# Performance work log

Hardware: AMD Instinct MI355X
Metric: run time of the kernel (lower is better)

## Reference

```python
import jax, jax.numpy as jnp
import numpy as np
import math

B, H, S, D = 2, 8, 1024, 384
LAMBDA_INIT = 0.8 - 0.6 * math.exp(-0.3 * 1)  # depth = 1


def _clin(xr, xi, wr, wi, br=None, bi=None):
    # complex linear: (xr + i xi) @ (wr + i wi)^T + (br + i bi)
    o_r = jnp.einsum('bhse,de->bhsd', xr, wr) - jnp.einsum('bhse,de->bhsd', xi, wi)
    o_i = jnp.einsum('bhse,de->bhsd', xr, wi) + jnp.einsum('bhse,de->bhsd', xi, wr)
    if br is not None:
        o_r = o_r + br
        o_i = o_i + bi
    return o_r, o_i


def _attn_w(qr, qi, kr, ki, scale):
    # complex score magnitude -> softmax
    s_r = jnp.einsum('bhqd,bhkd->bhqk', qr, kr) + jnp.einsum('bhqd,bhkd->bhqk', qi, ki)
    s_i = jnp.einsum('bhqd,bhkd->bhqk', qi, kr) - jnp.einsum('bhqd,bhkd->bhqk', qr, ki)
    return jax.nn.softmax(jnp.sqrt(s_r ** 2 + s_i ** 2 + 1e-8) * scale, axis=-1)


def setup_inputs() -> dict:
    key = jax.random.key(0)
    ks = jax.random.split(key, 32)
    n = lambda k, sh, std=1.0: jax.random.normal(k, sh, dtype=jnp.float32) * std
    sd = 1.0 / math.sqrt(D)
    inp = {
        'q_r': n(ks[0], (B, H, S, D)), 'q_i': n(ks[1], (B, H, S, D)),
        'k_r': n(ks[2], (B, H, S, D)), 'k_i': n(ks[3], (B, H, S, D)),
        'v_r': n(ks[4], (B, H, S, D)), 'v_i': n(ks[5], (B, H, S, D)),
        'pe_q_r': n(ks[6], (B, H, S, D)), 'pe_q_i': n(ks[7], (B, H, S, D)),
        'pe_k_r': n(ks[8], (B, H, S, D)), 'pe_k_i': n(ks[9], (B, H, S, D)),
        'wq_r': n(ks[10], (2 * D, D), sd), 'wq_i': n(ks[11], (2 * D, D), sd),
        'bq_r': jnp.zeros((2 * D,), jnp.float32), 'bq_i': jnp.zeros((2 * D,), jnp.float32),
        'wk_r': n(ks[12], (D, D), sd), 'wk_i': n(ks[13], (D, D), sd),
        'bk_r': jnp.zeros((D,), jnp.float32), 'bk_i': jnp.zeros((D,), jnp.float32),
        'wv_r': n(ks[14], (D, D), sd), 'wv_i': n(ks[15], (D, D), sd),
        'bv_r': jnp.zeros((D,), jnp.float32), 'bv_i': jnp.zeros((D,), jnp.float32),
        'wg_r': n(ks[16], (D, D), sd), 'wg_i': n(ks[17], (D, D), sd),
        'bg_r': jnp.zeros((D,), jnp.float32), 'bg_i': jnp.zeros((D,), jnp.float32),
        'wo_r': n(ks[18], (D, D), sd), 'wo_i': n(ks[19], (D, D), sd),
        'bo_r': jnp.zeros((D,), jnp.float32), 'bo_i': jnp.zeros((D,), jnp.float32),
        'lam_q1': n(ks[20], (D,), 0.1), 'lam_k1': n(ks[21], (D,), 0.1),
        'lam_q2': n(ks[22], (D,), 0.1), 'lam_k2': n(ks[23], (D,), 0.1),
        'subln_w': jnp.ones((2 * D,), jnp.float32),
    }
    return inp


def reference(q_r, q_i, k_r, k_i, v_r, v_i, pe_q_r, pe_q_i, pe_k_r, pe_k_i,
              wq_r, wq_i, bq_r, bq_i, wk_r, wk_i, bk_r, bk_i,
              wv_r, wv_i, bv_r, bv_i, wg_r, wg_i, bg_r, bg_i,
              wo_r, wo_i, bo_r, bo_i, lam_q1, lam_k1, lam_q2, lam_k2, subln_w):
    scale = D ** (-0.5)
    qp_r, qp_i = _clin(q_r, q_i, wq_r, wq_i, bq_r, bq_i)   # [B,H,S,2D]
    kp_r, kp_i = _clin(k_r, k_i, wk_r, wk_i, bk_r, bk_i)   # [B,H,S,D]
    vp_r, vp_i = _clin(v_r, v_i, wv_r, wv_i, bv_r, bv_i)
    qp_r = qp_r + jnp.concatenate([pe_q_r, pe_q_r], axis=-1)
    qp_i = qp_i + jnp.concatenate([pe_q_i, pe_q_i], axis=-1)
    kp_r = kp_r + pe_k_r
    kp_i = kp_i + pe_k_i
    q1_r, q2_r = jnp.split(qp_r, 2, axis=-1)
    q1_i, q2_i = jnp.split(qp_i, 2, axis=-1)
    w1 = _attn_w(q1_r, q1_i, kp_r, kp_i, scale)
    w2 = _attn_w(q2_r, q2_i, kp_r, kp_i, scale)
    a1_r = jnp.einsum('bhqk,bhkd->bhqd', w1, vp_r)
    a1_i = jnp.einsum('bhqk,bhkd->bhqd', w1, vp_i)
    a2_r = jnp.einsum('bhqk,bhkd->bhqd', w2, vp_r)
    a2_i = jnp.einsum('bhqk,bhkd->bhqd', w2, vp_i)
    cat_r = jnp.concatenate([a1_r, a2_r], axis=-1)
    cat_i = jnp.concatenate([a1_i, a2_i], axis=-1)
    # complex RMSNorm (SubLN) over 2D dim
    rms = jnp.sqrt(jnp.mean(cat_r ** 2 + cat_i ** 2, axis=-1, keepdims=True) + 1e-5)
    cat_r = cat_r / rms * subln_w
    cat_i = cat_i / rms * subln_w
    a1_r, a2_r = jnp.split(cat_r, 2, axis=-1)
    a1_i, a2_i = jnp.split(cat_i, 2, axis=-1)
    lam1 = jnp.exp(jnp.sum(lam_q1 * lam_k1))
    lam2 = jnp.exp(jnp.sum(lam_q2 * lam_k2))
    lam = jax.nn.sigmoid(lam1 - lam2 + LAMBDA_INIT)
    out_r = a1_r - lam * a2_r
    out_i = a1_i - lam * a2_i
    g_r, g_i = _clin(q_r, q_i, wg_r, wg_i, bg_r, bg_i)
    out_r, out_i = g_r * out_r - g_i * out_i, g_r * out_i + g_i * out_r
    out_r, out_i = _clin(out_r, out_i, wo_r, wo_i, bo_r, bo_i)
    return (out_r, out_i)
```

## Files before the change

kernel.cpp:

```cpp
#include <hip/hip_runtime.h>
#include <cstdint>


typedef _Float16 f16;
typedef __attribute__((ext_vector_type(8))) _Float16 f16x8;
typedef __attribute__((ext_vector_type(4))) float    f32x4;

#define NROW      16384L
#define HALF_OUT  6291456L
#define SCALE_QK  0.05103103630798288f
#define LAMBDA_INIT 0.35550906759096926f

__device__ __forceinline__ void gl2lds16(const void* g, void* l) {
  __builtin_amdgcn_global_load_lds(
      (const __attribute__((address_space(1))) void*)(uintptr_t)g,
      (__attribute__((address_space(3))) void*)(uint32_t)(uintptr_t)l,
      16, 0, 0);
}

struct PeTab { const float* p[6]; float sgn[6]; };

enum { MODE_PROJ = 0, MODE_VT = 1, MODE_OUT = 2 };

template <int MODE, int BN>
__launch_bounds__(256, 2)
__global__ void gemm_kernel(const f16* __restrict__ A, int lda,
                            const f16* __restrict__ W, int ldw,
                            const float* __restrict__ bias, PeTab pe,
                            void* __restrict__ outp, int ldo, int K)
{
  constexpr int NT = BN / 32;
  __shared__ f16 As[2][128 * 32];
  __shared__ f16 Bs[2][BN * 32];
  const int t    = threadIdx.x;
  const int lane = t & 63;
  const int wave = t >> 6;
  const long row0 = (long)blockIdx.y * 128;
  const long col0 = (long)blockIdx.x * BN;
  const f16* Ab = A + row0 * (long)lda;
  const f16* Wb = W + col0 * (long)ldw;

  const int wm = (wave >> 1) * 64;
  const int wn = (wave & 1) * (BN / 2);
  const int lm = lane & 15;
  const int lk = (lane >> 4) * 8;

  f32x4 acc[4][NT] = {};

  auto stage = [&](int kk, int buf) {
#pragma unroll
    for (int j = 0; j < 2; ++j) {
      int sg = j * 256 + t, r = sg >> 2, c = (sg & 3) << 3;
      gl2lds16(Ab + (long)r * lda + kk + c, &As[buf][sg * 8]);
    }
#pragma unroll
    for (int j = 0; j < BN / 64; ++j) {
      int sg = j * 256 + t, r = sg >> 2, c = (sg & 3) << 3;
      gl2lds16(Wb + (long)r * ldw + kk + c, &Bs[buf][sg * 8]);
    }
  };

  stage(0, 0);
  __syncthreads();
  int buf = 0;
  for (int kk = 0; kk < K; kk += 32, buf ^= 1) {
    if (kk + 32 < K) stage(kk + 32, buf ^ 1);
    f16x8 bfr[NT];
#pragma unroll
    for (int nt = 0; nt < NT; ++nt)
      bfr[nt] = *(const f16x8*)&Bs[buf][(wn + nt * 16 + lm) * 32 + lk];
#pragma unroll
    for (int mt = 0; mt < 4; ++mt) {
      f16x8 afr = *(const f16x8*)&As[buf][(wm + mt * 16 + lm) * 32 + lk];
#pragma unroll
      for (int nt = 0; nt < NT; ++nt)
        acc[mt][nt] = __builtin_amdgcn_mfma_f32_16x16x32_f16(afr, bfr[nt], acc[mt][nt], 0, 0, 0);
    }
    __syncthreads();
  }

  const int lm4 = (lane >> 4) * 4;
  const int ln  = lane & 15;
#pragma unroll
  for (int mt = 0; mt < 4; ++mt) {
#pragma unroll
    for (int nt = 0; nt < NT; ++nt) {
      int col = (int)col0 + wn + nt * 16 + ln;
#pragma unroll
      for (int r = 0; r < 4; ++r) {
        long row = row0 + wm + mt * 16 + lm4 + r;
        float c = acc[mt][nt][r];
        if (MODE == MODE_PROJ) {
          c += bias[col];
          int s2 = col / 384;
          int d  = col - s2 * 384;
          const float* pp = pe.p[s2];
          if (pp) c += pe.sgn[s2] * pp[row * 384 + d];
          ((f16*)outp)[row * (long)ldo + col] = (f16)c;
        } else if (MODE == MODE_VT) {
          c += bias[col];
          long bh = row >> 10, sx = row & 1023;
          ((f16*)outp)[(bh * 768 + col) * 1024 + sx] = (f16)c;
        } else {
          c += bias[col];
          float* of = (float*)outp;
          if (col < 384) of[row * 384 + col] = c;
          else           of[HALF_OUT + row * 384 + (col - 384)] = c;
        }
      }
    }
  }
}

__launch_bounds__(256, 2)
__global__ void score_kernel(const f16* __restrict__ QG, const f16* __restrict__ Kc,
                             f16* __restrict__ P)
{
  __shared__ f16 AsL[2][128 * 32], AsH[2][128 * 32];
  __shared__ f16 BsL[2][128 * 32], BsH[2][128 * 32];
  const int t = threadIdx.x, lane = t & 63, wave = t >> 6;
  const int z = blockIdx.z, w = z >> 4, bh = z & 15;
  const long row0 = (long)blockIdx.y * 128, col0 = (long)blockIdx.x * 128;
  const f16* A = QG + (long)bh * 1024 * 2304 + row0 * 2304 + w * 768;
  const f16* B = Kc + (long)bh * 1024 * 768 + col0 * 768;
  f16* Pz = P + (long)z * 1024 * 1024;

  const int wm = (wave >> 1) * 64, wn = (wave & 1) * 64;
  const int lm = lane & 15, lk = (lane >> 4) * 8;
  f32x4 accr[4][4] = {}, acci[4][4] = {};

  auto stage = [&](int kk, int buf) {
#pragma unroll
    for (int j = 0; j < 2; ++j) {
      int sg = j * 256 + t, r = sg >> 2, c = (sg & 3) << 3;
      gl2lds16(A + (long)r * 2304 + kk + c,       &AsL[buf][sg * 8]);
      gl2lds16(A + (long)r * 2304 + 384 + kk + c, &AsH[buf][sg * 8]);
      gl2lds16(B + (long)r * 768 + kk + c,        &BsL[buf][sg * 8]);
      gl2lds16(B + (long)r * 768 + 384 + kk + c,  &BsH[buf][sg * 8]);
    }
  };

  stage(0, 0);
  __syncthreads();
  int buf = 0;
  for (int kk = 0; kk < 384; kk += 32, buf ^= 1) {
    if (kk + 32 < 384) stage(kk + 32, buf ^ 1);
    f16x8 bl[4], bh2[4];
#pragma unroll
    for (int nt = 0; nt < 4; ++nt) {
      bl[nt]  = *(const f16x8*)&BsL[buf][(wn + nt * 16 + lm) * 32 + lk];
      bh2[nt] = *(const f16x8*)&BsH[buf][(wn + nt * 16 + lm) * 32 + lk];
    }
#pragma unroll
    for (int mt = 0; mt < 4; ++mt) {
      f16x8 al  = *(const f16x8*)&AsL[buf][(wm + mt * 16 + lm) * 32 + lk];
      f16x8 ah  = *(const f16x8*)&AsH[buf][(wm + mt * 16 + lm) * 32 + lk];
      f16x8 nal = -al;
#pragma unroll
      for (int nt = 0; nt < 4; ++nt) {
        accr[mt][nt] = __builtin_amdgcn_mfma_f32_16x16x32_f16(al,  bl[nt],  accr[mt][nt], 0, 0, 0);
        accr[mt][nt] = __builtin_amdgcn_mfma_f32_16x16x32_f16(ah,  bh2[nt], accr[mt][nt], 0, 0, 0);
        acci[mt][nt] = __builtin_amdgcn_mfma_f32_16x16x32_f16(ah,  bl[nt],  acci[mt][nt], 0, 0, 0);
        acci[mt][nt] = __builtin_amdgcn_mfma_f32_16x16x32_f16(nal, bh2[nt], acci[mt][nt], 0, 0, 0);
      }
    }
    __syncthreads();
  }
  const int lm4 = (lane >> 4) * 4, ln = lane & 15;
#pragma unroll
  for (int mt = 0; mt < 4; ++mt)
#pragma unroll
    for (int nt = 0; nt < 4; ++nt) {
      int col = (int)col0 + wn + nt * 16 + ln;
#pragma unroll
      for (int r = 0; r < 4; ++r) {
        long row = row0 + wm + mt * 16 + lm4 + r;
        float sr = accr[mt][nt][r], si = acci[mt][nt][r];
        float m = sqrtf(sr * sr + si * si + 1e-8f) * SCALE_QK;
        Pz[row * 1024 + col] = (f16)m;
      }
    }
}

__launch_bounds__(256, 2)
__global__ void pv_kernel(const f16* __restrict__ P, const f16* __restrict__ Vt,
                          f16* __restrict__ O1, f16* __restrict__ O2)
{
  __shared__ f16 As1[2][128 * 32], As2[2][128 * 32], Bs[2][128 * 32];
  const int t = threadIdx.x, lane = t & 63, wave = t >> 6;
  const int bh = blockIdx.z;
  const long row0 = (long)blockIdx.y * 128, col0 = (long)blockIdx.x * 128;
  const f16* A1 = P + ((long)bh << 20) + row0 * 1024;
  const f16* A2 = P + ((long)(16 + bh) << 20) + row0 * 1024;
  const f16* B  = Vt + (long)bh * 768 * 1024 + col0 * 1024;

  const int wm = (wave >> 1) * 64, wn = (wave & 1) * 64;
  const int lm = lane & 15, lk = (lane >> 4) * 8;
  f32x4 ac1[4][4] = {}, ac2[4][4] = {};

  auto stage = [&](int kk, int buf) {
#pragma unroll
    for (int j = 0; j < 2; ++j) {
      int sg = j * 256 + t, r = sg >> 2, c = (sg & 3) << 3;
      gl2lds16(A1 + (long)r * 1024 + kk + c, &As1[buf][sg * 8]);
      gl2lds16(A2 + (long)r * 1024 + kk + c, &As2[buf][sg * 8]);
      gl2lds16(B  + (long)r * 1024 + kk + c, &Bs[buf][sg * 8]);
    }
  };

  stage(0, 0);
  __syncthreads();
  int buf = 0;
  for (int kk = 0; kk < 1024; kk += 32, buf ^= 1) {
    if (kk + 32 < 1024) stage(kk + 32, buf ^ 1);
    f16x8 bfr[4];
#pragma unroll
    for (int nt = 0; nt < 4; ++nt)
      bfr[nt] = *(const f16x8*)&Bs[buf][(wn + nt * 16 + lm) * 32 + lk];
#pragma unroll
    for (int mt = 0; mt < 4; ++mt) {
      f16x8 a1 = *(const f16x8*)&As1[buf][(wm + mt * 16 + lm) * 32 + lk];
      f16x8 a2 = *(const f16x8*)&As2[buf][(wm + mt * 16 + lm) * 32 + lk];
#pragma unroll
      for (int nt = 0; nt < 4; ++nt) {
        ac1[mt][nt] = __builtin_amdgcn_mfma_f32_16x16x32_f16(a1, bfr[nt], ac1[mt][nt], 0, 0, 0);
        ac2[mt][nt] = __builtin_amdgcn_mfma_f32_16x16x32_f16(a2, bfr[nt], ac2[mt][nt], 0, 0, 0);
      }
    }
    __syncthreads();
  }
  const int lm4 = (lane >> 4) * 4, ln = lane & 15;
#pragma unroll
  for (int mt = 0; mt < 4; ++mt)
#pragma unroll
    for (int nt = 0; nt < 4; ++nt) {
      int col = (int)col0 + wn + nt * 16 + ln;
#pragma unroll
      for (int r = 0; r < 4; ++r) {
        long row = (long)bh * 1024 + row0 + wm + mt * 16 + lm4 + r;
        O1[row * 768 + col] = (f16)ac1[mt][nt][r];
        O2[row * 768 + col] = (f16)ac2[mt][nt][r];
      }
    }
}

__global__ void softmax_kernel(f16* __restrict__ P)
{
  const long row = blockIdx.x;
  f16* p = P + row * 1024;
  const int lane = threadIdx.x;
  f16x8 v0 = *(const f16x8*)(p + lane * 16);
  f16x8 v1 = *(const f16x8*)(p + lane * 16 + 8);
  float x[16];
#pragma unroll
  for (int i = 0; i < 8; ++i) { x[i] = (float)v0[i]; x[8 + i] = (float)v1[i]; }
  float m = x[0];
#pragma unroll
  for (int i = 1; i < 16; ++i) m = fmaxf(m, x[i]);
#pragma unroll
  for (int off = 1; off < 64; off <<= 1) m = fmaxf(m, __shfl_xor(m, off));
  float s = 0.f;
#pragma unroll
  for (int i = 0; i < 16; ++i) { x[i] = __expf(x[i] - m); s += x[i]; }
#pragma unroll
  for (int off = 1; off < 64; off <<= 1) s += __shfl_xor(s, off);
  float inv = 1.f / s;
  f16x8 o0, o1;
#pragma unroll
  for (int i = 0; i < 8; ++i) { o0[i] = (f16)(x[i] * inv); o1[i] = (f16)(x[8 + i] * inv); }
  *(f16x8*)(p + lane * 16)     = o0;
  *(f16x8*)(p + lane * 16 + 8) = o1;
}

__global__ void fuse_kernel(const f16* __restrict__ A1, const f16* __restrict__ A2,
                            const f16* __restrict__ QG, const float* __restrict__ subw,
                            const float* __restrict__ lamp, f16* __restrict__ Xatt)
{
  const long row = blockIdx.x;
  const int t = threadIdx.x, lane = t & 63, wv = t >> 6;
  const f16* a1 = A1 + row * 768;
  const f16* a2 = A2 + row * 768;
  const f16* g  = QG + row * 2304 + 1536;
  float a1r[3], a1i[3], a2r[3], a2i[3];
  float ss = 0.f;
#pragma unroll
  for (int q = 0; q < 3; ++q) {
    int d = t + q * 128;
    a1r[q] = (float)a1[d]; a1i[q] = (float)a1[d + 384];
    a2r[q] = (float)a2[d]; a2i[q] = (float)a2[d + 384];
    ss += a1r[q] * a1r[q] + a1i[q] * a1i[q] + a2r[q] * a2r[q] + a2i[q] * a2i[q];
  }
#pragma unroll
  for (int m = 1; m < 64; m <<= 1) ss += __shfl_xor(ss, m);
  __shared__ float part[2];
  if (lane == 0) part[wv] = ss;
  __syncthreads();
  float inv = rsqrtf((part[0] + part[1]) * (1.f / 768.f) + 1e-5f);
  float lam = lamp[0];
#pragma unroll
  for (int q = 0; q < 3; ++q) {
    int d = t + q * 128;
    float w1 = subw[d], w2 = subw[d + 384];
    float n1r = a1r[q] * inv * w1, n1i = a1i[q] * inv * w1;
    float n2r = a2r[q] * inv * w2, n2i = a2i[q] * inv * w2;
    float orr = n1r - lam * n2r, oii = n1i - lam * n2i;
    float gr = (float)g[d], gi = (float)g[d + 384];
    Xatt[row * 768 + d]       = (f16)(gr * orr - gi * oii);
    Xatt[row * 768 + d + 384] = (f16)(gr * oii + gi * orr);
  }
}

__global__ void lam_kernel(const float* lq1, const float* lk1,
                           const float* lq2, const float* lk2, float* out)
{
  const int t = threadIdx.x, lane = t & 63, wv = t >> 6;
  float s1 = 0.f, s2 = 0.f;
#pragma unroll
  for (int q = 0; q < 3; ++q) {
    int d = t + q * 128;
    s1 += lq1[d] * lk1[d];
    s2 += lq2[d] * lk2[d];
  }
#pragma unroll
  for (int m = 1; m < 64; m <<= 1) { s1 += __shfl_xor(s1, m); s2 += __shfl_xor(s2, m); }
  __shared__ float p1[2], p2[2];
  if (lane == 0) { p1[wv] = s1; p2[wv] = s2; }
  __syncthreads();
  if (t == 0) {
    float x = expf(p1[0] + p1[1]) - expf(p2[0] + p2[1]) + LAMBDA_INIT;
    out[0] = 1.f / (1.f + expf(-x));
  }
}

__global__ void pack_x(const float* __restrict__ xr, const float* __restrict__ xi,
                       f16* __restrict__ X)
{
  long i = (long)blockIdx.x * 256 + threadIdx.x;
  long row = i / 768;
  int  c   = (int)(i - row * 768);
  float v = (c < 384) ? xr[row * 384 + c] : xi[row * 384 + (c - 384)];
  X[i] = (f16)v;
}

__global__ void pack_wq(const float* wq_r, const float* wq_i,
                        const float* wg_r, const float* wg_i,
                        const float* bq_r, const float* bq_i,
                        const float* bg_r, const float* bg_i,
                        f16* __restrict__ Wp, float* __restrict__ bp)
{
  long i = (long)blockIdx.x * 256 + threadIdx.x;
  int n = (int)(i / 768), e = (int)(i % 768);
  int s = n / 384, d = n - s * 384;
  int hb = (e >= 384);
  int ee = e - hb * 384;
  float v = 0.f, b = 0.f;
  switch (s) {
    case 0: v = hb ? -wq_i[d * 384 + ee]         :  wq_r[d * 384 + ee];         b = bq_r[d];       break;
    case 1: v = hb ?  wq_r[d * 384 + ee]         :  wq_i[d * 384 + ee];         b = bq_i[d];       break;
    case 2: v = hb ? -wq_i[(384 + d) * 384 + ee] :  wq_r[(384 + d) * 384 + ee]; b = bq_r[384 + d]; break;
    case 3: v = hb ?  wq_r[(384 + d) * 384 + ee] :  wq_i[(384 + d) * 384 + ee]; b = bq_i[384 + d]; break;
    case 4: v = hb ? -wg_i[d * 384 + ee]         :  wg_r[d * 384 + ee];         b = bg_r[d];       break;
    case 5: v = hb ?  wg_r[d * 384 + ee]         :  wg_i[d * 384 + ee];         b = bg_i[d];       break;
  }
  Wp[i] = (f16)v;
  if (e == 0) bp[n] = b;
}

__global__ void pack_w_std(const float* wr, const float* wi,
                           const float* br, const float* bi,
                           f16* __restrict__ Wp, float* __restrict__ bp)
{
  long i = (long)blockIdx.x * 256 + threadIdx.x;
  int n = (int)(i / 768), e = (int)(i % 768);
  int hb = (e >= 384);
  int ee = e - hb * 384;
  float v, b;
  if (n < 384) { v = hb ? -wi[n * 384 + ee] : wr[n * 384 + ee]; b = br[n]; }
  else { int d = n - 384; v = hb ? wr[d * 384 + ee] : wi[d * 384 + ee]; b = bi[d]; }
  Wp[i] = (f16)v;
  if (e == 0) bp[n] = b;
}

extern "C" void kernel_launch(void* const* d_in, const int* in_sizes, int n_in,
                              void* d_out, int out_size, void* d_ws, size_t ws_size,
                              hipStream_t stream)
{
  const float* q_r    = (const float*)d_in[0];
  const float* q_i    = (const float*)d_in[1];
  const float* k_r    = (const float*)d_in[2];
  const float* k_i    = (const float*)d_in[3];
  const float* v_r    = (const float*)d_in[4];
  const float* v_i    = (const float*)d_in[5];
  const float* pe_q_r = (const float*)d_in[6];
  const float* pe_q_i = (const float*)d_in[7];
  const float* pe_k_r = (const float*)d_in[8];
  const float* pe_k_i = (const float*)d_in[9];
  const float* wq_r = (const float*)d_in[10];
  const float* wq_i = (const float*)d_in[11];
  const float* bq_r = (const float*)d_in[12];
  const float* bq_i = (const float*)d_in[13];
  const float* wk_r = (const float*)d_in[14];
  const float* wk_i = (const float*)d_in[15];
  const float* bk_r = (const float*)d_in[16];
  const float* bk_i = (const float*)d_in[17];
  const float* wv_r = (const float*)d_in[18];
  const float* wv_i = (const float*)d_in[19];
  const float* bv_r = (const float*)d_in[20];
  const float* bv_i = (const float*)d_in[21];
  const float* wg_r = (const float*)d_in[22];
  const float* wg_i = (const float*)d_in[23];
  const float* bg_r = (const float*)d_in[24];
  const float* bg_i = (const float*)d_in[25];
  const float* wo_r = (const float*)d_in[26];
  const float* wo_i = (const float*)d_in[27];
  const float* bo_r = (const float*)d_in[28];
  const float* bo_i = (const float*)d_in[29];
  const float* lam_q1 = (const float*)d_in[30];
  const float* lam_k1 = (const float*)d_in[31];
  const float* lam_q2 = (const float*)d_in[32];
  const float* lam_k2 = (const float*)d_in[33];
  const float* subln_w = (const float*)d_in[34];

  char* base = (char*)d_ws;
  size_t off = 0;
  auto alloc = [&](size_t bytes) -> void* {
    void* p = base + off;
    off = (off + bytes + 255) & ~(size_t)255;
    return p;
  };
  f16*   Wq   = (f16*)alloc(2304L * 768 * 2);
  f16*   Wk   = (f16*)alloc(768L * 768 * 2);
  f16*   Wv   = (f16*)alloc(768L * 768 * 2);
  f16*   Wo   = (f16*)alloc(768L * 768 * 2);
  float* bq   = (float*)alloc(2304 * 4);
  float* bk   = (float*)alloc(768 * 4);
  float* bv   = (float*)alloc(768 * 4);
  float* bo   = (float*)alloc(768 * 4);
  float* lamp = (float*)alloc(4);
  f16*   X    = (f16*)alloc(NROW * 768 * 2);
  f16*   QG   = (f16*)alloc(NROW * 2304 * 2);
  f16*   Kc   = (f16*)alloc(NROW * 768 * 2);
  f16*   Vt   = (f16*)alloc(16L * 768 * 1024 * 2);
  f16*   P    = (f16*)alloc(32L * 1024 * 1024 * 2);
  if (off > ws_size) return;
  f16* A1   = Kc;
  f16* A2   = X;
  f16* Xatt = Vt;

  pack_wq<<<6912, 256, 0, stream>>>(wq_r, wq_i, wg_r, wg_i, bq_r, bq_i, bg_r, bg_i, Wq, bq);
  pack_w_std<<<2304, 256, 0, stream>>>(wk_r, wk_i, bk_r, bk_i, Wk, bk);
  pack_w_std<<<2304, 256, 0, stream>>>(wv_r, wv_i, bv_r, bv_i, Wv, bv);
  pack_w_std<<<2304, 256, 0, stream>>>(wo_r, wo_i, bo_r, bo_i, Wo, bo);
  lam_kernel<<<1, 128, 0, stream>>>(lam_q1, lam_k1, lam_q2, lam_k2, lamp);

  PeTab pe0{};

  pack_x<<<49152, 256, 0, stream>>>(q_r, q_i, X);
  PeTab peQ{};
  peQ.p[0] = pe_q_r; peQ.sgn[0] = 1.f;
  peQ.p[1] = pe_q_i; peQ.sgn[1] = 1.f;
  peQ.p[2] = pe_q_r; peQ.sgn[2] = 1.f;
  peQ.p[3] = pe_q_i; peQ.sgn[3] = 1.f;
  gemm_kernel<MODE_PROJ, 256><<<dim3(9, 128), 256, 0, stream>>>(
      X, 768, Wq, 768, bq, peQ, QG, 2304, 768);

  pack_x<<<49152, 256, 0, stream>>>(k_r, k_i, X);
  PeTab peK{};
  peK.p[0] = pe_k_r; peK.sgn[0] = 1.f;
  peK.p[1] = pe_k_i; peK.sgn[1] = 1.f;
  gemm_kernel<MODE_PROJ, 128><<<dim3(6, 128), 256, 0, stream>>>(
      X, 768, Wk, 768, bk, peK, Kc, 768, 768);

  pack_x<<<49152, 256, 0, stream>>>(v_r, v_i, X);
  gemm_kernel<MODE_VT, 128><<<dim3(6, 128), 256, 0, stream>>>(
      X, 768, Wv, 768, bv, pe0, Vt, 0, 768);

  score_kernel<<<dim3(8, 8, 32), 256, 0, stream>>>(QG, Kc, P);
  softmax_kernel<<<32768, 64, 0, stream>>>(P);
  pv_kernel<<<dim3(6, 8, 16), 256, 0, stream>>>(P, Vt, A1, A2);

  fuse_kernel<<<16384, 128, 0, stream>>>(A1, A2, QG, subln_w, lamp, Xatt);

  gemm_kernel<MODE_OUT, 128><<<dim3(6, 128), 256, 0, stream>>>(
      Xatt, 768, Wo, 768, bo, pe0, d_out, 0, 768);

  (void)in_sizes; (void)n_in; (void)out_size;
}
```

Baseline: 900.3 us.

## Remap GEMM blocks to XCDs for L2 locality and restructure K-loop staging

After: 833.8 us. 7.4% less time.

```diff
diff --git a/kernel.cpp b/kernel.cpp
--- a/kernel.cpp
+++ b/kernel.cpp
@@ -4,6 +4,7 @@
 
 typedef _Float16 f16;
 typedef __attribute__((ext_vector_type(8))) _Float16 f16x8;
+typedef __attribute__((ext_vector_type(4))) _Float16 f16x4;
 typedef __attribute__((ext_vector_type(4))) float    f32x4;
 
 #define NROW      16384L
@@ -22,59 +23,59 @@
 
 enum { MODE_PROJ = 0, MODE_VT = 1, MODE_OUT = 2 };
 
-template <int MODE, int BN>
+template <int MODE>
 __launch_bounds__(256, 2)
 __global__ void gemm_kernel(const f16* __restrict__ A, int lda,
                             const f16* __restrict__ W, int ldw,
                             const float* __restrict__ bias, PeTab pe,
-                            void* __restrict__ outp, int ldo, int K)
-{
-  constexpr int NT = BN / 32;
+                            void* __restrict__ outp, int ldo, int K, int gx)
+{
   __shared__ f16 As[2][128 * 32];
-  __shared__ f16 Bs[2][BN * 32];
+  __shared__ f16 Bs[2][128 * 32];
   const int t    = threadIdx.x;
   const int lane = t & 63;
   const int wave = t >> 6;
-  const long row0 = (long)blockIdx.y * 128;
-  const long col0 = (long)blockIdx.x * BN;
+  const int bid  = blockIdx.x;
+  const int xcd  = bid & 7;
+  const int per  = bid >> 3;
+  const long row0 = (long)(xcd * 16 + per / gx) * 128;
+  const long col0 = (long)(per % gx) * 128;
   const f16* Ab = A + row0 * (long)lda;
   const f16* Wb = W + col0 * (long)ldw;
 
   const int wm = (wave >> 1) * 64;
-  const int wn = (wave & 1) * (BN / 2);
+  const int wn = (wave & 1) * 64;
   const int lm = lane & 15;
   const int lk = (lane >> 4) * 8;
 
-  f32x4 acc[4][NT] = {};
-
-  auto stage = [&](int kk, int buf) {
+  f32x4 acc[4][4] = {};
+
+  auto stage = [&](int kk, int sub) {
 #pragma unroll
     for (int j = 0; j < 2; ++j) {
       int sg = j * 256 + t, r = sg >> 2, c = (sg & 3) << 3;
-      gl2lds16(Ab + (long)r * lda + kk + c, &As[buf][sg * 8]);
-    }
-#pragma unroll
-    for (int j = 0; j < BN / 64; ++j) {
-      int sg = j * 256 + t, r = sg >> 2, c = (sg & 3) << 3;
-      gl2lds16(Wb + (long)r * ldw + kk + c, &Bs[buf][sg * 8]);
+      gl2lds16(Ab + (long)r * lda + kk + c, &As[sub][sg * 8]);
+      gl2lds16(Wb + (long)r * ldw + kk + c, &Bs[sub][sg * 8]);
     }
   };
 
-  stage(0, 0);
-  __syncthreads();
-  int buf = 0;
-  for (int kk = 0; kk < K; kk += 32, buf ^= 1) {
-    if (kk + 32 < K) stage(kk + 32, buf ^ 1);
-    f16x8 bfr[NT];
-#pragma unroll
-    for (int nt = 0; nt < NT; ++nt)
-      bfr[nt] = *(const f16x8*)&Bs[buf][(wn + nt * 16 + lm) * 32 + lk];
-#pragma unroll
-    for (int mt = 0; mt < 4; ++mt) {
-      f16x8 afr = *(const f16x8*)&As[buf][(wm + mt * 16 + lm) * 32 + lk];
-#pragma unroll
-      for (int nt = 0; nt < NT; ++nt)
-        acc[mt][nt] = __builtin_amdgcn_mfma_f32_16x16x32_f16(afr, bfr[nt], acc[mt][nt], 0, 0, 0);
+  for (int kk = 0; kk < K; kk += 64) {
+    stage(kk, 0);
+    stage(kk + 32, 1);
+    __syncthreads();
+#pragma unroll
+    for (int sub = 0; sub < 2; ++sub) {
+      f16x8 bfr[4];
+#pragma unroll
+      for (int nt = 0; nt < 4; ++nt)
+        bfr[nt] = *(const f16x8*)&Bs[sub][(wn + nt * 16 + lm) * 32 + lk];
+#pragma unroll
+      for (int mt = 0; mt < 4; ++mt) {
+        f16x8 afr = *(const f16x8*)&As[sub][(wm + mt * 16 + lm) * 32 + lk];
+#pragma unroll
+        for (int nt = 0; nt < 4; ++nt)
+          acc[mt][nt] = __builtin_amdgcn_mfma_f32_16x16x32_f16(afr, bfr[nt], acc[mt][nt], 0, 0, 0);
+      }
     }
     __syncthreads();
   }
@@ -84,28 +85,31 @@
 #pragma unroll
   for (int mt = 0; mt < 4; ++mt) {
 #pragma unroll
-    for (int nt = 0; nt < NT; ++nt) {
+    for (int nt = 0; nt < 4; ++nt) {
       int col = (int)col0 + wn + nt * 16 + ln;
-#pragma unroll
-      for (int r = 0; r < 4; ++r) {
-        long row = row0 + wm + mt * 16 + lm4 + r;
-        float c = acc[mt][nt][r];
-        if (MODE == MODE_PROJ) {
-          c += bias[col];
-          int s2 = col / 384;
-          int d  = col - s2 * 384;
-          const float* pp = pe.p[s2];
-          if (pp) c += pe.sgn[s2] * pp[row * 384 + d];
-          ((f16*)outp)[row * (long)ldo + col] = (f16)c;
-        } else if (MODE == MODE_VT) {
-          c += bias[col];
-          long bh = row >> 10, sx = row & 1023;
-          ((f16*)outp)[(bh * 768 + col) * 1024 + sx] = (f16)c;
-        } else {
-          c += bias[col];
-          float* of = (float*)outp;
-          if (col < 384) of[row * 384 + col] = c;
-          else           of[HALF_OUT + row * 384 + (col - 384)] = c;
+      if (MODE == MODE_VT) {
+        long rowb = row0 + wm + mt * 16 + lm4;
+        long bh = rowb >> 10, sx = rowb & 1023;
+        f16x4 v;
+#pragma unroll
+        for (int r = 0; r < 4; ++r) v[r] = (f16)(acc[mt][nt][r] + bias[col]);
+        *(f16x4*)&((f16*)outp)[(bh * 768 + col) * 1024 + sx] = v;
+      } else {
+#pragma unroll
+        for (int r = 0; r < 4; ++r) {
+          long row = row0 + wm + mt * 16 + lm4 + r;
+          float c = acc[mt][nt][r] + bias[col];
+          if (MODE == MODE_PROJ) {
+            int s2 = col / 384;
+            int d  = col - s2 * 384;
+            const float* pp = pe.p[s2];
+            if (pp) c += pe.sgn[s2] * pp[row * 384 + d];
+            ((f16*)outp)[row * (long)ldo + col] = (f16)c;
+          } else {
+            float* of = (float*)outp;
+            if (col < 384) of[row * 384 + col] = c;
+            else           of[HALF_OUT + row * 384 + (col - 384)] = c;
+          }
         }
       }
     }
@@ -116,11 +120,14 @@
 __global__ void score_kernel(const f16* __restrict__ QG, const f16* __restrict__ Kc,
                              f16* __restrict__ P)
 {
-  __shared__ f16 AsL[2][128 * 32], AsH[2][128 * 32];
-  __shared__ f16 BsL[2][128 * 32], BsH[2][128 * 32];
+  __shared__ f16 AsL[128 * 32], AsH[128 * 32], BsL[128 * 32], BsH[128 * 32];
   const int t = threadIdx.x, lane = t & 63, wave = t >> 6;
-  const int z = blockIdx.z, w = z >> 4, bh = z & 15;
-  const long row0 = (long)blockIdx.y * 128, col0 = (long)blockIdx.x * 128;
+  const int bid = blockIdx.x;
+  const int xcd = bid & 7, per = bid >> 3;
+  const int z   = xcd * 4 + per / 64;
+  const int rem = per % 64;
+  const int w = z >> 4, bh = z & 15;
+  const long row0 = (long)(rem / 8) * 128, col0 = (long)(rem % 8) * 128;
   const f16* A = QG + (long)bh * 1024 * 2304 + row0 * 2304 + w * 768;
   const f16* B = Kc + (long)bh * 1024 * 768 + col0 * 768;
   f16* Pz = P + (long)z * 1024 * 1024;
@@ -129,32 +136,26 @@
   const int lm = lane & 15, lk = (lane >> 4) * 8;
   f32x4 accr[4][4] = {}, acci[4][4] = {};
 
-  auto stage = [&](int kk, int buf) {
+  for (int kk = 0; kk < 384; kk += 32) {
 #pragma unroll
     for (int j = 0; j < 2; ++j) {
       int sg = j * 256 + t, r = sg >> 2, c = (sg & 3) << 3;
-      gl2lds16(A + (long)r * 2304 + kk + c,       &AsL[buf][sg * 8]);
-      gl2lds16(A + (long)r * 2304 + 384 + kk + c, &AsH[buf][sg * 8]);
-      gl2lds16(B + (long)r * 768 + kk + c,        &BsL[buf][sg * 8]);
-      gl2lds16(B + (long)r * 768 + 384 + kk + c,  &BsH[buf][sg * 8]);
-    }
-  };
-
-  stage(0, 0);
-  __syncthreads();
-  int buf = 0;
-  for (int kk = 0; kk < 384; kk += 32, buf ^= 1) {
-    if (kk + 32 < 384) stage(kk + 32, buf ^ 1);
+      gl2lds16(A + (long)r * 2304 + kk + c,       &AsL[sg * 8]);
+      gl2lds16(A + (long)r * 2304 + 384 + kk + c, &AsH[sg * 8]);
+      gl2lds16(B + (long)r * 768 + kk + c,        &BsL[sg * 8]);
+      gl2lds16(B + (long)r * 768 + 384 + kk + c,  &BsH[sg * 8]);
+    }
+    __syncthreads();
     f16x8 bl[4], bh2[4];
 #pragma unroll
     for (int nt = 0; nt < 4; ++nt) {
-      bl[nt]  = *(const f16x8*)&BsL[buf][(wn + nt * 16 + lm) * 32 + lk];
-      bh2[nt] = *(const f16x8*)&BsH[buf][(wn + nt * 16 + lm) * 32 + lk];
+      bl[nt]  = *(const f16x8*)&BsL[(wn + nt * 16 + lm) * 32 + lk];
+      bh2[nt] = *(const f16x8*)&BsH[(wn + nt * 16 + lm) * 32 + lk];
     }
 #pragma unroll
     for (int mt = 0; mt < 4; ++mt) {
-      f16x8 al  = *(const f16x8*)&AsL[buf][(wm + mt * 16 + lm) * 32 + lk];
-      f16x8 ah  = *(const f16x8*)&AsH[buf][(wm + mt * 16 + lm) * 32 + lk];
+      f16x8 al  = *(const f16x8*)&AsL[(wm + mt * 16 + lm) * 32 + lk];
+      f16x8 ah  = *(const f16x8*)&AsH[(wm + mt * 16 + lm) * 32 + lk];
       f16x8 nal = -al;
 #pragma unroll
       for (int nt = 0; nt < 4; ++nt) {
@@ -188,8 +189,11 @@
 {
   __shared__ f16 As1[2][128 * 32], As2[2][128 * 32], Bs[2][128 * 32];
   const int t = threadIdx.x, lane = t & 63, wave = t >> 6;
-  const int bh = blockIdx.z;
-  const long row0 = (long)blockIdx.y * 128, col0 = (long)blockIdx.x * 128;
+  const int bid = blockIdx.x;
+  const int xcd = bid & 7, per = bid >> 3;
+  const int bh  = xcd * 2 + per / 48;
+  const int rem = per % 48;
+  const long row0 = (long)(rem / 6) * 128, col0 = (long)(rem % 6) * 128;
   const f16* A1 = P + ((long)bh << 20) + row0 * 1024;
   const f16* A2 = P + ((long)(16 + bh) << 20) + row0 * 1024;
   const f16* B  = Vt + (long)bh * 768 * 1024 + col0 * 1024;
@@ -198,33 +202,35 @@
   const int lm = lane & 15, lk = (lane >> 4) * 8;
   f32x4 ac1[4][4] = {}, ac2[4][4] = {};
 
-  auto stage = [&](int kk, int buf) {
+  auto stage = [&](int kk, int sub) {
 #pragma unroll
     for (int j = 0; j < 2; ++j) {
       int sg = j * 256 + t, r = sg >> 2, c = (sg & 3) << 3;
-      gl2lds16(A1 + (long)r * 1024 + kk + c, &As1[buf][sg * 8]);
-      gl2lds16(A2 + (long)r * 1024 + kk + c, &As2[buf][sg * 8]);
-      gl2lds16(B  + (long)r * 1024 + kk + c, &Bs[buf][sg * 8]);
+      gl2lds16(A1 + (long)r * 1024 + kk + c, &As1[sub][sg * 8]);
+      gl2lds16(A2 + (long)r * 1024 + kk + c, &As2[sub][sg * 8]);
+      gl2lds16(B  + (long)r * 1024 + kk + c, &Bs[sub][sg * 8]);
     }
   };
 
-  stage(0, 0);
-  __syncthreads();
-  int buf = 0;
-  for (int kk = 0; kk < 1024; kk += 32, buf ^= 1) {
-    if (kk + 32 < 1024) stage(kk + 32, buf ^ 1);
-    f16x8 bfr[4];
-#pragma unroll
-    for (int nt = 0; nt < 4; ++nt)
-      bfr[nt] = *(const f16x8*)&Bs[buf][(wn + nt * 16 + lm) * 32 + lk];
-#pragma unroll
-    for (int mt = 0; mt < 4; ++mt) {
-      f16x8 a1 = *(const f16x8*)&As1[buf][(wm + mt * 16 + lm) * 32 + lk];
-      f16x8 a2 = *(const f16x8*)&As2[buf][(wm + mt * 16 + lm) * 32 + lk];
-#pragma unroll
-      for (int nt = 0; nt < 4; ++nt) {
-        ac1[mt][nt] = __builtin_amdgcn_mfma_f32_16x16x32_f16(a1, bfr[nt], ac1[mt][nt], 0, 0, 0);
-        ac2[mt][nt] = __builtin_amdgcn_mfma_f32_16x16x32_f16(a2, bfr[nt], ac2[mt][nt], 0, 0, 0);
+  for (int kk = 0; kk < 1024; kk += 64) {
+    stage(kk, 0);
+    stage(kk + 32, 1);
+    __syncthreads();
+#pragma unroll
+    for (int sub = 0; sub < 2; ++sub) {
+      f16x8 bfr[4];
+#pragma unroll
+      for (int nt = 0; nt < 4; ++nt)
+        bfr[nt] = *(const f16x8*)&Bs[sub][(wn + nt * 16 + lm) * 32 + lk];
+#pragma unroll
+      for (int mt = 0; mt < 4; ++mt) {
+        f16x8 a1 = *(const f16x8*)&As1[sub][(wm + mt * 16 + lm) * 32 + lk];
+        f16x8 a2 = *(const f16x8*)&As2[sub][(wm + mt * 16 + lm) * 32 + lk];
+#pragma unroll
+        for (int nt = 0; nt < 4; ++nt) {
+          ac1[mt][nt] = __builtin_amdgcn_mfma_f32_16x16x32_f16(a1, bfr[nt], ac1[mt][nt], 0, 0, 0);
+          ac2[mt][nt] = __builtin_amdgcn_mfma_f32_16x16x32_f16(a2, bfr[nt], ac2[mt][nt], 0, 0, 0);
+        }
       }
     }
     __syncthreads();
@@ -461,28 +467,28 @@
   peQ.p[1] = pe_q_i; peQ.sgn[1] = 1.f;
   peQ.p[2] = pe_q_r; peQ.sgn[2] = 1.f;
   peQ.p[3] = pe_q_i; peQ.sgn[3] = 1.f;
-  gemm_kernel<MODE_PROJ, 256><<<dim3(9, 128), 256, 0, stream>>>(
-      X, 768, Wq, 768, bq, peQ, QG, 2304, 768);
+  gemm_kernel<MODE_PROJ><<<2304, 256, 0, stream>>>(
+      X, 768, Wq, 768, bq, peQ, QG, 2304, 768, 18);
 
   pack_x<<<49152, 256, 0, stream>>>(k_r, k_i, X);
   PeTab peK{};
   peK.p[0] = pe_k_r; peK.sgn[0] = 1.f;
   peK.p[1] = pe_k_i; peK.sgn[1] = 1.f;
-  gemm_kernel<MODE_PROJ, 128><<<dim3(6, 128), 256, 0, stream>>>(
-      X, 768, Wk, 768, bk, peK, Kc, 768, 768);
+  gemm_kernel<MODE_PROJ><<<768, 256, 0, stream>>>(
+      X, 768, Wk, 768, bk, peK, Kc, 768, 768, 6);
 
   pack_x<<<49152, 256, 0, stream>>>(v_r, v_i, X);
-  gemm_kernel<MODE_VT, 128><<<dim3(6, 128), 256, 0, stream>>>(
-      X, 768, Wv, 768, bv, pe0, Vt, 0, 768);
-
-  score_kernel<<<dim3(8, 8, 32), 256, 0, stream>>>(QG, Kc, P);
+  gemm_kernel<MODE_VT><<<768, 256, 0, stream>>>(
+      X, 768, Wv, 768, bv, pe0, Vt, 0, 768, 6);
+
+  score_kernel<<<2048, 256, 0, stream>>>(QG, Kc, P);
   softmax_kernel<<<32768, 64, 0, stream>>>(P);
-  pv_kernel<<<dim3(6, 8, 16), 256, 0, stream>>>(P, Vt, A1, A2);
+  pv_kernel<<<768, 256, 0, stream>>>(P, Vt, A1, A2);
 
   fuse_kernel<<<16384, 128, 0, stream>>>(A1, A2, QG, subln_w, lamp, Xatt);
 
-  gemm_kernel<MODE_OUT, 128><<<dim3(6, 128), 256, 0, stream>>>(
-      Xatt, 768, Wo, 768, bo, pe0, d_out, 0, 768);
+  gemm_kernel<MODE_OUT><<<768, 256, 0, stream>>>(
+      Xatt, 768, Wo, 768, bo, pe0, d_out, 0, 768, 6);
 
   (void)in_sizes; (void)n_in; (void)out_size;
 }
```
